# Performance work log

Measured on AMD Instinct MI355X. Metric: run time of the kernel, lower is better.

Reference implementation:

```python
import jax, jax.numpy as jnp
import numpy as np

EPS = 1e-5
H = 1024  # hidden_size
IN = 1024  # input_size
B = 4096


def _layer_norm(x, gamma, beta):
    mu = jnp.mean(x, axis=-1, keepdims=True)
    var = jnp.mean(jnp.square(x - mu), axis=-1, keepdims=True)
    return (x - mu) * jax.lax.rsqrt(var + EPS) * gamma + beta


def setup_inputs() -> dict:
    key = jax.random.key(0)
    ks = jax.random.split(key, 8)
    s_h = 1.0 / np.sqrt(H)
    s_x = 1.0 / np.sqrt(IN)
    return {
        "x": jax.random.normal(ks[0], (B, IN), dtype=jnp.float32),
        "h": jax.random.normal(ks[1], (B, H), dtype=jnp.float32),
        "c": jax.random.normal(ks[2], (B, H), dtype=jnp.float32),
        # hidden_lin: Linear(H, 4H) with bias; input_lin: Linear(IN, 4H) no bias
        "W_h": jax.random.uniform(ks[3], (H, 4 * H), jnp.float32, -s_h, s_h),
        "b_h": jax.random.uniform(ks[4], (4 * H,), jnp.float32, -s_h, s_h),
        "W_x": jax.random.uniform(ks[5], (IN, 4 * H), jnp.float32, -s_x, s_x),
        # 4 gate LayerNorms stacked [4,H], plus LayerNorm for c
        "ln_g": jnp.ones((4, H), jnp.float32),
        "ln_b": jnp.zeros((4, H), jnp.float32),
        "lnc_g": jnp.ones((H,), jnp.float32),
        "lnc_b": jnp.zeros((H,), jnp.float32),
    }


def reference(x, h, c, W_h, b_h, W_x, ln_g, ln_b, lnc_g, lnc_b):
    # ifgo = hidden_lin(h) + input_lin(x) : [B, 4H]
    ifgo = h @ W_h + b_h + x @ W_x
    ifgo = ifgo.reshape(x.shape[0], 4, H)  # [B, 4, H]
    ifgo = _layer_norm(ifgo, ln_g, ln_b)   # per-gate LayerNorm over last dim
    i, f, g, o = ifgo[:, 0], ifgo[:, 1], ifgo[:, 2], ifgo[:, 3]
    c_next = jax.nn.sigmoid(f) * c + jax.nn.sigmoid(i) * jnp.tanh(g)
    h_next = jax.nn.sigmoid(o) * jnp.tanh(_layer_norm(c_next, lnc_g, lnc_b))
    return (h_next, c_next)
```

## Files before the change

kernel.cpp:

```cpp
#include <hip/hip_runtime.h>

typedef short bf16x8 __attribute__((ext_vector_type(8)));
typedef unsigned short u16x8 __attribute__((ext_vector_type(8)));
typedef float f32x4  __attribute__((ext_vector_type(4)));

__device__ __forceinline__ float bf2f(unsigned short u) {
  union { unsigned int i; float f; } x; x.i = ((unsigned int)u) << 16; return x.f;
}
__device__ __forceinline__ unsigned short f2bf(float f) {
  union { float f; unsigned int i; } x; x.f = f;
  unsigned int r = x.i + 0x7fffu + ((x.i >> 16) & 1u);
  return (unsigned short)(r >> 16);
}
__device__ __forceinline__ float sigm(float v) { return 1.f / (1.f + __expf(-v)); }
__device__ __forceinline__ float tanh_(float v) { return 1.f - 2.f / (__expf(2.f * v) + 1.f); }
__device__ __forceinline__ int is_fp32(const void* lng) {
  return ((*(const unsigned int*)lng) & 0xFFFFu) == 0u;
}

#define AS1 __attribute__((address_space(1)))
#define AS3 __attribute__((address_space(3)))

__global__ __launch_bounds__(256) void prep_kernel(
    const void* __restrict__ h, const void* __restrict__ x,
    const void* __restrict__ Wh, const void* __restrict__ Wx,
    const void* __restrict__ lng,
    unsigned short* __restrict__ Ap, unsigned short* __restrict__ Wt)
{
  __shared__ __align__(16) unsigned short tkn[64][64];
  const int fp = is_fp32(lng);
  const int bid = blockIdx.x;
  const int t = threadIdx.x;

#pragma unroll
  for (int i = 0; i < 2; ++i) {
    const int row = bid * 2 + i;
    const int col = t * 8;
    const void* srcA; int sc;
    if (col < 1024) { srcA = h; sc = col; } else { srcA = x; sc = col - 1024; }
    u16x8 o;
    if (fp) {
      const float* s = (const float*)srcA + (size_t)row * 1024 + sc;
      float4 a4 = *(const float4*)s;
      float4 b4 = *(const float4*)(s + 4);
      o[0] = f2bf(a4.x); o[1] = f2bf(a4.y); o[2] = f2bf(a4.z); o[3] = f2bf(a4.w);
      o[4] = f2bf(b4.x); o[5] = f2bf(b4.y); o[6] = f2bf(b4.z); o[7] = f2bf(b4.w);
    } else {
      o = *(const u16x8*)((const unsigned short*)srcA + (size_t)row * 1024 + sc);
    }
    *(u16x8*)(Ap + (size_t)row * 2048 + col) = o;
  }

  const int n0 = (bid & 63) * 64;
  const int k0 = (bid >> 6) * 64;
  const void* src; int krow;
  if (k0 < 1024) { src = Wh; krow = k0; } else { src = Wx; krow = k0 - 1024; }
  if (fp) {
#pragma unroll
    for (int i = 0; i < 4; ++i) {
      const int k  = (t >> 4) + i * 16;
      const int n4 = (t & 15) * 4;
      float4 w = *(const float4*)((const float*)src + (size_t)(krow + k) * 4096 + n0 + n4);
      ushort4 u; u.x = f2bf(w.x); u.y = f2bf(w.y); u.z = f2bf(w.z); u.w = f2bf(w.w);
      *(ushort4*)&tkn[k][n4] = u;
    }
  } else {
#pragma unroll
    for (int i = 0; i < 2; ++i) {
      const int k  = (t >> 3) + i * 32;
      const int n8 = (t & 7) * 8;
      *(u16x8*)&tkn[k][n8] =
          *(const u16x8*)((const unsigned short*)src + (size_t)(krow + k) * 4096 + n0 + n8);
    }
  }
  __syncthreads();
#pragma unroll
  for (int i = 0; i < 2; ++i) {
    const int n  = (t >> 3) + i * 32;
    const int k8 = (t & 7) * 8;
    u16x8 o;
#pragma unroll
    for (int j = 0; j < 8; ++j) o[j] = tkn[k8 + j][n];
    *(u16x8*)(Wt + (size_t)(n0 + n) * 2048 + k0 + k8) = o;
  }
}

#define BAR()   __builtin_amdgcn_s_barrier()
#define VMW(N)  { asm volatile("s_waitcnt vmcnt(" #N ")" ::: "memory"); }
#define LGKM0() { asm volatile("s_waitcnt lgkmcnt(0)" ::: "memory"); }

#define LOAD_A(DB, MH)                                                         \
  { const unsigned short* _ba = &As[DB][(MH)*128 + wr*64 + fr][0];             \
    _Pragma("unroll") for (int mi = 0; mi < 4; ++mi)                           \
      _Pragma("unroll") for (int kh = 0; kh < 2; ++kh)                         \
        a[mi][kh] = *(const bf16x8*)(_ba + mi*1024 + ((kh*4 + fq) ^ xk) * 8); }

#define LOAD_B(DB, NH, BT)                                                     \
  { const unsigned short* _bb = &Bs[DB][(NH)*128 + wc*32 + fr][0];             \
    _Pragma("unroll") for (int ni = 0; ni < 2; ++ni)                           \
      _Pragma("unroll") for (int kh = 0; kh < 2; ++kh)                         \
        (BT)[ni][kh] = *(const bf16x8*)(_bb + ni*1024 + ((kh*4 + fq) ^ xk) * 8); }

#define MFMA16(MH, NH, BT)                                                     \
  { __builtin_amdgcn_s_setprio(1);                                             \
    _Pragma("unroll") for (int kh = 0; kh < 2; ++kh)                           \
      _Pragma("unroll") for (int mi = 0; mi < 4; ++mi)                         \
        _Pragma("unroll") for (int ni = 0; ni < 2; ++ni)                       \
          acc[MH][mi][NH][ni] = __builtin_amdgcn_mfma_f32_16x16x32_bf16(       \
              a[mi][kh], (BT)[ni][kh], acc[MH][mi][NH][ni], 0, 0, 0);          \
    __builtin_amdgcn_s_setprio(0); }

#define STAGE(G, LDS, ROW0, H, KT)                                             \
  { _Pragma("unroll") for (int l = 0; l < 2; ++l) {                            \
      const int _idx = l * 512 + tid;                                          \
      const int _r = _idx >> 3;                                                \
      const int _sg = (_idx & 7) ^ (_r & 7);                                   \
      const unsigned short* _src = (G) + (size_t)((ROW0) + (H)*128 + _r) * 2048\
                                   + ((KT) << 6) + _sg * 8;                    \
      __builtin_amdgcn_global_load_lds((const AS1 void*)_src,                  \
          (AS3 void*)(&(LDS)[0][0] + (H)*8192 + (l*512 + wave*64)*8), 16, 0, 0);\
  } }

__global__ __launch_bounds__(512, 2) void gemm_kernel(
    const unsigned short* __restrict__ Ap,
    const unsigned short* __restrict__ Wt,
    unsigned short* __restrict__ Cout)
{
  __shared__ __align__(16) unsigned short As[2][256][64];
  __shared__ __align__(16) unsigned short Bs[2][256][64];

  const int bid = blockIdx.x;
  const int swz = (bid & 7) * 32 + (bid >> 3);
  const int bm = swz >> 4, bn = swz & 15;
  const int arow = bm * 256, brow = bn * 256;

  const int tid  = threadIdx.x;
  const int wave = tid >> 6, lane = tid & 63;
  const int wr = wave >> 2, wc = wave & 3;
  const int fr = lane & 15, fq = lane >> 4;
  const int xk = fr & 7;

  f32x4 acc[2][4][2][2] = {};
  bf16x8 a[4][2], bA[2][2], bB[2][2];

  STAGE(Wt, Bs[0], brow, 0, 0);
  STAGE(Ap, As[0], arow, 0, 0);
  STAGE(Wt, Bs[0], brow, 1, 0);
  STAGE(Ap, As[0], arow, 1, 0);
  STAGE(Wt, Bs[1], brow, 0, 1);
  STAGE(Ap, As[1], arow, 0, 1);
  STAGE(Wt, Bs[1], brow, 1, 1);
  STAGE(Ap, As[1], arow, 1, 1);
  VMW(8);
  BAR();
  LOAD_B(0, 0, bA)
  LGKM0();

#pragma unroll 1
  for (int it = 0; it < 16; ++it) {
    const int t2 = (2 * it + 2) & 31;
    const int t3 = (2 * it + 3) & 31;

    LOAD_A(0, 0)
    STAGE(Wt, Bs[0], brow, 0, t2);
    BAR();
    MFMA16(0, 0, bA);
    BAR();
    LOAD_B(0, 1, bB)
    STAGE(Ap, As[0], arow, 0, t2);
    BAR();
    MFMA16(0, 1, bB);
    BAR();
    LOAD_A(0, 1)
    STAGE(Wt, Bs[0], brow, 1, t2);
    BAR();
    MFMA16(1, 1, bB);
    BAR();
    VMW(6);
    LOAD_B(1, 0, bB)
    STAGE(Ap, As[0], arow, 1, t2);
    BAR();
    MFMA16(1, 0, bA);
    LGKM0();
    BAR();
    LOAD_A(1, 0)
    STAGE(Wt, Bs[1], brow, 0, t3);
    BAR();
    MFMA16(0, 0, bB);
    BAR();
    LOAD_B(1, 1, bA)
    STAGE(Ap, As[1], arow, 0, t3);
    BAR();
    MFMA16(0, 1, bA);
    BAR();
    LOAD_A(1, 1)
    STAGE(Wt, Bs[1], brow, 1, t3);
    BAR();
    MFMA16(1, 1, bA);
    BAR();
    VMW(6);
    LOAD_B(0, 0, bA)
    STAGE(Ap, As[1], arow, 1, t3);
    BAR();
    MFMA16(1, 0, bB);
    LGKM0();
    BAR();
  }
  VMW(0);

  unsigned short* Cb = Cout + (size_t)arow * 4096 + brow;
#pragma unroll
  for (int mh = 0; mh < 2; ++mh)
#pragma unroll
    for (int mi = 0; mi < 4; ++mi)
#pragma unroll
      for (int nh = 0; nh < 2; ++nh)
#pragma unroll
        for (int ni = 0; ni < 2; ++ni) {
          const int row = mh * 128 + wr * 64 + mi * 16 + fq * 4;
          const int col = nh * 128 + wc * 32 + ni * 16 + fr;
#pragma unroll
          for (int r = 0; r < 4; ++r)
            Cb[(size_t)(row + r) * 4096 + col] = f2bf(acc[mh][mi][nh][ni][r]);
        }
}

__device__ __forceinline__ float4 load4(const void* p, size_t idx, int fp) {
  if (fp) return *(const float4*)((const float*)p + idx);
  ushort4 u = *(const ushort4*)((const unsigned short*)p + idx);
  return make_float4(bf2f(u.x), bf2f(u.y), bf2f(u.z), bf2f(u.w));
}
__device__ __forceinline__ void store4(void* p, size_t idx, int fp,
                                       float a, float b, float c, float d) {
  if (fp) {
    *(float4*)((float*)p + idx) = make_float4(a, b, c, d);
  } else {
    ushort4 u; u.x = f2bf(a); u.y = f2bf(b); u.z = f2bf(c); u.w = f2bf(d);
    *(ushort4*)((unsigned short*)p + idx) = u;
  }
}

__global__ __launch_bounds__(256) void ln_lstm_kernel(
    const unsigned short* __restrict__ parts,
    const void* __restrict__ c,
    const void* __restrict__ bh,
    const void* __restrict__ ln_g,
    const void* __restrict__ ln_b,
    const void* __restrict__ lnc_g,
    const void* __restrict__ lnc_b,
    void* __restrict__ out)
{
  const int t = threadIdx.x;
  const int lane = t & 63, wave = t >> 6;
  const int fp = is_fp32(lnc_g);

  __shared__ float sred[4][8];

  float4 bias4[4];
#pragma unroll
  for (int q = 0; q < 4; ++q) bias4[q] = load4(bh, q * 1024 + t * 4, fp);
  float gg[4][4], gb[4][4];
#pragma unroll
  for (int q = 0; q < 4; ++q) {
    float4 g4 = load4(ln_g, q * 1024 + t * 4, fp);
    float4 b4 = load4(ln_b, q * 1024 + t * 4, fp);
    gg[q][0] = g4.x; gg[q][1] = g4.y; gg[q][2] = g4.z; gg[q][3] = g4.w;
    gb[q][0] = b4.x; gb[q][1] = b4.y; gb[q][2] = b4.z; gb[q][3] = b4.w;
  }
  float4 cg4 = load4(lnc_g, t * 4, fp);
  float4 cb4 = load4(lnc_b, t * 4, fp);
  float cgv[4] = { cg4.x, cg4.y, cg4.z, cg4.w };
  float cbv[4] = { cb4.x, cb4.y, cb4.z, cb4.w };

#pragma unroll 1
  for (int r = 0; r < 4; ++r) {
    const int b = blockIdx.x * 4 + r;
    const unsigned short* P0 = parts + (size_t)b * 4096;
    __syncthreads();

    float v[4][4];
    float red[8];
#pragma unroll
    for (int q = 0; q < 4; ++q) {
      ushort4 p0 = *(const ushort4*)(P0 + q * 1024 + t * 4);
      v[q][0] = bf2f(p0.x) + bias4[q].x;
      v[q][1] = bf2f(p0.y) + bias4[q].y;
      v[q][2] = bf2f(p0.z) + bias4[q].z;
      v[q][3] = bf2f(p0.w) + bias4[q].w;
      red[q * 2]     = v[q][0] + v[q][1] + v[q][2] + v[q][3];
      red[q * 2 + 1] = v[q][0]*v[q][0] + v[q][1]*v[q][1] + v[q][2]*v[q][2] + v[q][3]*v[q][3];
    }
#pragma unroll
    for (int j = 0; j < 8; ++j) {
      float s = red[j];
#pragma unroll
      for (int off = 32; off > 0; off >>= 1) s += __shfl_down(s, off, 64);
      if (lane == 0) sred[wave][j] = s;
    }
    __syncthreads();
    float mu[4], rs[4];
#pragma unroll
    for (int q = 0; q < 4; ++q) {
      float s  = sred[0][2*q]   + sred[1][2*q]   + sred[2][2*q]   + sred[3][2*q];
      float sq = sred[0][2*q+1] + sred[1][2*q+1] + sred[2][2*q+1] + sred[3][2*q+1];
      mu[q] = s * (1.f / 1024.f);
      float var = sq * (1.f / 1024.f) - mu[q] * mu[q];
      rs[q] = rsqrtf(var + 1e-5f);
    }

    float4 c4 = load4(c, (size_t)b * 1024 + t * 4, fp);
    float cin[4] = { c4.x, c4.y, c4.z, c4.w };

    float cn[4], osg[4];
    float csum = 0.f, csq = 0.f;
#pragma unroll
    for (int e = 0; e < 4; ++e) {
      float iv = (v[0][e] - mu[0]) * rs[0] * gg[0][e] + gb[0][e];
      float fv = (v[1][e] - mu[1]) * rs[1] * gg[1][e] + gb[1][e];
      float gv = (v[2][e] - mu[2]) * rs[2] * gg[2][e] + gb[2][e];
      float ov = (v[3][e] - mu[3]) * rs[3] * gg[3][e] + gb[3][e];
      float cne = sigm(fv) * cin[e] + sigm(iv) * tanh_(gv);
      cn[e] = cne; csum += cne; csq += cne * cne;
      osg[e] = sigm(ov);
    }
    store4(out, (size_t)4096 * 1024 + (size_t)b * 1024 + t * 4, fp, cn[0], cn[1], cn[2], cn[3]);

    __syncthreads();
    {
      float s0 = csum, s1 = csq;
#pragma unroll
      for (int off = 32; off > 0; off >>= 1) { s0 += __shfl_down(s0, off, 64); s1 += __shfl_down(s1, off, 64); }
      if (lane == 0) { sred[wave][0] = s0; sred[wave][1] = s1; }
    }
    __syncthreads();
    float cs   = sred[0][0] + sred[1][0] + sred[2][0] + sred[3][0];
    float csq2 = sred[0][1] + sred[1][1] + sred[2][1] + sred[3][1];
    float mu_c = cs * (1.f / 1024.f);
    float var_c = csq2 * (1.f / 1024.f) - mu_c * mu_c;
    float rs_c = rsqrtf(var_c + 1e-5f);

    float hn[4];
#pragma unroll
    for (int e = 0; e < 4; ++e)
      hn[e] = osg[e] * tanh_((cn[e] - mu_c) * rs_c * cgv[e] + cbv[e]);
    store4(out, (size_t)b * 1024 + t * 4, fp, hn[0], hn[1], hn[2], hn[3]);
  }
}

extern "C" void kernel_launch(void* const* d_in, const int* in_sizes, int n_in,
                              void* d_out, int out_size, void* d_ws, size_t ws_size,
                              hipStream_t stream) {
  const void* x    = d_in[0];
  const void* h    = d_in[1];
  const void* c    = d_in[2];
  const void* Wh   = d_in[3];
  const void* bh   = d_in[4];
  const void* Wx   = d_in[5];
  const void* lng  = d_in[6];
  const void* lnb  = d_in[7];
  const void* lncg = d_in[8];
  const void* lncb = d_in[9];

  char* ws = (char*)d_ws;
  unsigned short* parts = (unsigned short*)ws;
  unsigned short* Wt    = (unsigned short*)(ws + (size_t)64 * 1024 * 1024);
  unsigned short* Ap    = (unsigned short*)(ws + (size_t)80 * 1024 * 1024);

  prep_kernel<<<2048, 256, 0, stream>>>(h, x, Wh, Wx, lng, Ap, Wt);
  gemm_kernel<<<dim3(256), 512, 0, stream>>>(Ap, Wt, parts);
  ln_lstm_kernel<<<1024, 256, 0, stream>>>(parts, c, bh, lng, lnb, lncg, lncb, d_out);
}
```

Before: 220.0 us.

## Restructure GEMM main loop into four phases with batched MFMA groups

Reorganizes the GEMM inner loop from eight small phases into four larger phases. Each phase loads A and both B halves, then issues two MFMA groups between barriers, so the kernel runs fewer barriers and longer MFMA bursts. The staging order and wait counts are reshuffled to match, and the explicit lgkmcnt waits are dropped. The risk is a correctness hazard from changed load and wait ordering, plus extra register pressure from holding both B fragments at once.

```diff
diff --git a/kernel.cpp b/kernel.cpp
--- a/kernel.cpp
+++ b/kernel.cpp
@@ -85,9 +85,9 @@
   }
 }
 
+
 #define BAR()   __builtin_amdgcn_s_barrier()
 #define VMW(N)  { asm volatile("s_waitcnt vmcnt(" #N ")" ::: "memory"); }
-#define LGKM0() { asm volatile("s_waitcnt lgkmcnt(0)" ::: "memory"); }
 
 #define LOAD_A(DB, MH)                                                         \
   { const unsigned short* _ba = &As[DB][(MH)*128 + wr*64 + fr][0];             \
@@ -102,13 +102,11 @@
         (BT)[ni][kh] = *(const bf16x8*)(_bb + ni*1024 + ((kh*4 + fq) ^ xk) * 8); }
 
 #define MFMA16(MH, NH, BT)                                                     \
-  { __builtin_amdgcn_s_setprio(1);                                             \
-    _Pragma("unroll") for (int kh = 0; kh < 2; ++kh)                           \
+  { _Pragma("unroll") for (int kh = 0; kh < 2; ++kh)                           \
       _Pragma("unroll") for (int mi = 0; mi < 4; ++mi)                         \
         _Pragma("unroll") for (int ni = 0; ni < 2; ++ni)                       \
           acc[MH][mi][NH][ni] = __builtin_amdgcn_mfma_f32_16x16x32_bf16(       \
-              a[mi][kh], (BT)[ni][kh], acc[MH][mi][NH][ni], 0, 0, 0);          \
-    __builtin_amdgcn_s_setprio(0); }
+              a[mi][kh], (BT)[ni][kh], acc[MH][mi][NH][ni], 0, 0, 0); }
 
 #define STAGE(G, LDS, ROW0, H, KT)                                             \
   { _Pragma("unroll") for (int l = 0; l < 2; ++l) {                            \
@@ -141,69 +139,65 @@
   const int xk = fr & 7;
 
   f32x4 acc[2][4][2][2] = {};
-  bf16x8 a[4][2], bA[2][2], bB[2][2];
-
+  bf16x8 a[4][2], bB0[2][2], bB1[2][2];
+
+  STAGE(Ap, As[0], arow, 0, 0);
   STAGE(Wt, Bs[0], brow, 0, 0);
-  STAGE(Ap, As[0], arow, 0, 0);
   STAGE(Wt, Bs[0], brow, 1, 0);
   STAGE(Ap, As[0], arow, 1, 0);
+  STAGE(Ap, As[1], arow, 0, 1);
   STAGE(Wt, Bs[1], brow, 0, 1);
-  STAGE(Ap, As[1], arow, 0, 1);
   STAGE(Wt, Bs[1], brow, 1, 1);
-  STAGE(Ap, As[1], arow, 1, 1);
-  VMW(8);
+  VMW(6);
   BAR();
-  LOAD_B(0, 0, bA)
-  LGKM0();
 
 #pragma unroll 1
   for (int it = 0; it < 16; ++it) {
+    const int t1 = (2 * it + 1) & 31;
     const int t2 = (2 * it + 2) & 31;
     const int t3 = (2 * it + 3) & 31;
 
     LOAD_A(0, 0)
+    LOAD_B(0, 0, bB0)
+    LOAD_B(0, 1, bB1)
+    STAGE(Ap, As[1], arow, 1, t1);
+    BAR();
+    __builtin_amdgcn_s_setprio(1);
+    MFMA16(0, 0, bB0);
+    MFMA16(0, 1, bB1);
+    __builtin_amdgcn_s_setprio(0);
+    BAR();
+    LOAD_A(0, 1)
+    STAGE(Ap, As[0], arow, 0, t2);
     STAGE(Wt, Bs[0], brow, 0, t2);
-    BAR();
-    MFMA16(0, 0, bA);
-    BAR();
-    LOAD_B(0, 1, bB)
-    STAGE(Ap, As[0], arow, 0, t2);
-    BAR();
-    MFMA16(0, 1, bB);
-    BAR();
-    LOAD_A(0, 1)
     STAGE(Wt, Bs[0], brow, 1, t2);
     BAR();
-    MFMA16(1, 1, bB);
-    BAR();
+    __builtin_amdgcn_s_setprio(1);
+    MFMA16(1, 1, bB1);
+    MFMA16(1, 0, bB0);
+    __builtin_amdgcn_s_setprio(0);
     VMW(6);
-    LOAD_B(1, 0, bB)
+    BAR();
+    LOAD_A(1, 0)
+    LOAD_B(1, 0, bB0)
+    LOAD_B(1, 1, bB1)
     STAGE(Ap, As[0], arow, 1, t2);
     BAR();
-    MFMA16(1, 0, bA);
-    LGKM0();
-    BAR();
-    LOAD_A(1, 0)
+    __builtin_amdgcn_s_setprio(1);
+    MFMA16(0, 0, bB0);
+    MFMA16(0, 1, bB1);
+    __builtin_amdgcn_s_setprio(0);
+    BAR();
+    LOAD_A(1, 1)
+    STAGE(Ap, As[1], arow, 0, t3);
     STAGE(Wt, Bs[1], brow, 0, t3);
-    BAR();
-    MFMA16(0, 0, bB);
-    BAR();
-    LOAD_B(1, 1, bA)
-    STAGE(Ap, As[1], arow, 0, t3);
-    BAR();
-    MFMA16(0, 1, bA);
-    BAR();
-    LOAD_A(1, 1)
     STAGE(Wt, Bs[1], brow, 1, t3);
     BAR();
-    MFMA16(1, 1, bA);
-    BAR();
+    __builtin_amdgcn_s_setprio(1);
+    MFMA16(1, 1, bB1);
+    MFMA16(1, 0, bB0);
+    __builtin_amdgcn_s_setprio(0);
     VMW(6);
-    LOAD_B(0, 0, bA)
-    STAGE(Ap, As[1], arow, 1, t3);
-    BAR();
-    MFMA16(1, 0, bB);
-    LGKM0();
     BAR();
   }
   VMW(0);
```

After: 219.0 us. About the same (-0.5%).
